# Optimization experiments

Measured on AMD Instinct MI355X. Metric: run time of the kernel, lower is better.

Reference implementation:

```python
import jax, jax.numpy as jnp
import numpy as np
import math

B, N, C = 4, 2048, 768
H = 12
DFF = 4 * C
EPS = 1e-5

def _layernorm(x, gamma, beta):
    mu = jnp.mean(x, axis=-1, keepdims=True)
    var = jnp.var(x, axis=-1, keepdims=True)
    return (x - mu) * jax.lax.rsqrt(var + EPS) * gamma + beta

def setup_inputs() -> dict:
    key = jax.random.key(0)
    ks = jax.random.split(key, 12)
    s = 0.02
    return {
        "x": jax.random.normal(ks[0], (B, N, C), jnp.float32),
        "Wqkv": jax.random.normal(ks[1], (C, 3 * C), jnp.float32) * s,
        "bqkv": jnp.zeros((3 * C,), jnp.float32),
        "Wproj": jax.random.normal(ks[2], (C, C), jnp.float32) * s,
        "bproj": jnp.zeros((C,), jnp.float32),
        "g1": jnp.ones((C,), jnp.float32),
        "b1": jnp.zeros((C,), jnp.float32),
        "g2": jnp.ones((C,), jnp.float32),
        "b2": jnp.zeros((C,), jnp.float32),
        "Wfc1": jax.random.normal(ks[3], (C, DFF), jnp.float32) * s,
        "bfc1": jnp.zeros((DFF,), jnp.float32),
        "Wfc2": jax.random.normal(ks[4], (DFF, C), jnp.float32) * s,
        "bfc2": jnp.zeros((C,), jnp.float32),
    }

def reference(x, Wqkv, bqkv, Wproj, bproj, g1, b1, g2, b2, Wfc1, bfc1, Wfc2, bfc2):
    head_dim = C // H
    qkv = x @ Wqkv + bqkv                      # [B,N,3C]
    q, k, v = jnp.split(qkv, 3, axis=-1)
    # [B,N,C] -> [B,H,N,hd]
    def to_heads(t):
        return t.reshape(B, N, H, head_dim).transpose(0, 2, 1, 3)
    q, k, v = to_heads(q), to_heads(k), to_heads(v)
    attn = jnp.einsum('bhqd,bhkd->bhqk', q, k) / math.sqrt(head_dim)
    attn = jax.nn.softmax(attn, axis=-1)       # dropout p=0 -> identity
    out = jnp.einsum('bhqk,bhkd->bhqd', attn, v)
    out = out.transpose(0, 2, 1, 3).reshape(B, N, C)
    out = out @ Wproj + bproj
    x = _layernorm(x + out, g1, b1)
    h = jax.nn.gelu(x @ Wfc1 + bfc1, approximate=False) @ Wfc2 + bfc2
    x = _layernorm(x + h, g2, b2)
    return x
```

## Files before the change

### kernel.cpp

```cpp
#include <hip/hip_runtime.h>

typedef __bf16 bf16;
typedef __bf16 bf16x2 __attribute__((ext_vector_type(2)));
typedef __bf16 bf16x4 __attribute__((ext_vector_type(4)));
typedef __bf16 bf16x8 __attribute__((ext_vector_type(8)));
typedef float  f32x4  __attribute__((ext_vector_type(4)));
typedef float  f32x16 __attribute__((ext_vector_type(16)));
typedef int    intx4  __attribute__((ext_vector_type(4)));

#define BB 4
#define SEQ 2048
#define CH 768
#define NH 12
#define HD 64
#define DFF 3072
#define MROWS (BB * SEQ)
#define C3 (3 * CH)

__device__ inline f32x16 mfma32(bf16x8 a, bf16x8 b, f32x16 c) {
    return __builtin_amdgcn_mfma_f32_32x32x16_bf16(a, b, c, 0, 0, 0);
}
__device__ inline f32x4 mfma16(bf16x8 a, bf16x8 b, f32x4 c) {
    return __builtin_amdgcn_mfma_f32_16x16x32_bf16(a, b, c, 0, 0, 0);
}
__device__ inline void gload16(const void* g, void* l) {
    __builtin_amdgcn_global_load_lds((const __attribute__((address_space(1))) void*)g,
                                     (__attribute__((address_space(3))) void*)l, 16, 0, 0);
}

__global__ void cvt_f32_bf16(const float* __restrict__ in, bf16* __restrict__ out, int n) {
    int i = (blockIdx.x * blockDim.x + threadIdx.x) * 4;
    if (i + 3 >= n) {
        for (int j = 0; j < 4 && i + j < n; ++j) out[i + j] = (bf16)in[i + j];
        return;
    }
    f32x4 v = *(const f32x4*)&in[i];
    bf16x4 o;
    #pragma unroll
    for (int j = 0; j < 4; ++j) o[j] = (bf16)v[j];
    *(bf16x4*)&out[i] = o;
}

__global__ void transpose_cvt(const float* __restrict__ in, bf16* __restrict__ out, int R, int Cc) {
    __shared__ bf16 t[32][33];
    int tx = threadIdx.x & 31, ty = threadIdx.x >> 5;
    int c0 = blockIdx.x * 32, r0 = blockIdx.y * 32;
    #pragma unroll
    for (int i = 0; i < 32; i += 8)
        t[ty + i][tx] = (bf16)in[(size_t)(r0 + ty + i) * Cc + c0 + tx];
    __syncthreads();
    #pragma unroll
    for (int i = 0; i < 32; i += 8)
        out[(size_t)(c0 + ty + i) * R + r0 + tx] = t[tx][ty + i];
}

__global__ void transpose_v(const bf16* __restrict__ qkvb, bf16* __restrict__ vt) {
    __shared__ bf16 t[32][33];
    int tx = threadIdx.x & 31, ty = threadIdx.x >> 5;
    int n0 = blockIdx.x * 32, d0 = blockIdx.y * 32, bh = blockIdx.z;
    int b = bh / NH, h = bh - b * NH;
    #pragma unroll
    for (int i = 0; i < 32; i += 8)
        t[ty + i][tx] = qkvb[((size_t)b * SEQ + n0 + ty + i) * C3 + 2 * CH + h * HD + d0 + tx];
    __syncthreads();
    #pragma unroll
    for (int i = 0; i < 32; i += 8)
        vt[((size_t)bh * HD + d0 + ty + i) * SEQ + n0 + tx] = t[tx][ty + i];
}

template <int OMODE>
__global__ __launch_bounds__(256) void gemm_bt(const bf16* __restrict__ A,
                                               const bf16* __restrict__ Bt,
                                               const float* __restrict__ bias,
                                               void* __restrict__ Cout,
                                               int M, int N, int K, int lda) {
    __shared__ __align__(16) bf16 As[128][32];
    __shared__ __align__(16) bf16 Bs[128][32];
    const int nwg = gridDim.x * gridDim.y;
    const int orig = blockIdx.y * gridDim.x + blockIdx.x;
    const int wg = (orig & 7) * (nwg >> 3) + (orig >> 3);
    const int bm = (wg / gridDim.x) * 128, bn = (wg % gridDim.x) * 128;
    const int kbeg = blockIdx.z * K;
    const int tid = threadIdx.x;
    const int lane = tid & 63, w = tid >> 6;
    const int wr = w >> 1, wc = w & 1;
    const int lr = lane & 15, lg = lane >> 4;

    const int srow = tid >> 2, schk = (tid & 3) * 8;
    const bf16* gA0 = A + (size_t)(bm + srow) * lda + kbeg + schk;
    const bf16* gA1 = A + (size_t)(bm + 64 + srow) * lda + kbeg + schk;
    const bf16* gB0 = Bt + (size_t)(bn + srow) * lda + kbeg + schk;
    const bf16* gB1 = Bt + (size_t)(bn + 64 + srow) * lda + kbeg + schk;
    bf16* lA0 = &As[srow][schk];
    bf16* lA1 = &As[64 + srow][schk];
    bf16* lB0 = &Bs[srow][schk];
    bf16* lB1 = &Bs[64 + srow][schk];

    f32x4 acc[4][4];
    #pragma unroll
    for (int i = 0; i < 4; ++i)
        #pragma unroll
        for (int j = 0; j < 4; ++j) acc[i][j] = (f32x4){0.f, 0.f, 0.f, 0.f};

    for (int k0 = 0; k0 < K; k0 += 32) {
        __syncthreads();
        gload16(gA0, lA0); gload16(gA1, lA1);
        gload16(gB0, lB0); gload16(gB1, lB1);
        gA0 += 32; gA1 += 32; gB0 += 32; gB1 += 32;
        __syncthreads();
        bf16x8 af[4], bfr[4];
        #pragma unroll
        for (int mi = 0; mi < 4; ++mi)
            af[mi] = *(const bf16x8*)&As[wr * 64 + mi * 16 + lr][lg * 8];
        #pragma unroll
        for (int ni = 0; ni < 4; ++ni)
            bfr[ni] = *(const bf16x8*)&Bs[wc * 64 + ni * 16 + lr][lg * 8];
        #pragma unroll
        for (int mi = 0; mi < 4; ++mi)
            #pragma unroll
            for (int ni = 0; ni < 4; ++ni)
                acc[mi][ni] = mfma16(af[mi], bfr[ni], acc[mi][ni]);
    }

    float* outp = (float*)Cout;
    if (OMODE == 3) outp += (size_t)blockIdx.z * M * N;

    #pragma unroll
    for (int mi = 0; mi < 4; ++mi) {
        #pragma unroll
        for (int ni = 0; ni < 4; ++ni) {
            int col = bn + wc * 64 + ni * 16 + lr;
            float bsv = (OMODE == 3) ? 0.f : bias[col];
            #pragma unroll
            for (int r = 0; r < 4; ++r) {
                int row = bm + wr * 64 + mi * 16 + lg * 4 + r;
                float v = acc[mi][ni][r] + bsv;
                if (OMODE == 2) v = 0.5f * v * (1.0f + erff(v * 0.70710678118654752f));
                if (OMODE == 0 || OMODE == 3)
                    outp[(size_t)row * N + col] = v;
                else
                    ((bf16*)Cout)[(size_t)row * N + col] = (bf16)v;
            }
        }
    }
}

#define C2F 0.18033688011112f
#define THR2 11.5416f
__global__ __launch_bounds__(256, 3) void attn_kernel(const bf16* __restrict__ qkvb,
                                                      const bf16* __restrict__ vt,
                                                      bf16* __restrict__ outb) {
    __shared__ __align__(16) bf16 Kl[2][64 * 64];
    __shared__ __align__(16) bf16 Vl[2][64 * 64];
    const int tid = threadIdx.x;
    const int w = tid >> 6, lane = tid & 63;
    const int lq = lane & 31;
    const int hi = lane >> 5;
    const int lin = blockIdx.x;
    const int xcd = lin & 7, slot = lin >> 3;
    const int bh = xcd * 6 + (slot >> 4);
    const int qt = slot & 15;
    const int b = bh / NH, h = bh - b * NH;
    const int q0 = qt * 128 + w * 32;

    const bf16* qbase = qkvb + (size_t)b * SEQ * C3 + h * HD;
    const bf16* kbase = qbase + CH;
    const bf16* vbase = vt + (size_t)bh * HD * SEQ;

    const int srow = tid >> 3;
    const int ksc = (tid & 7) ^ (srow & 7);
    const bf16* gk0 = kbase + (size_t)srow * C3 + ksc * 8;
    const bf16* gk1 = kbase + (size_t)(srow + 32) * C3 + ksc * 8;
    const bf16* gv0 = vbase + (size_t)srow * SEQ + ksc * 8;
    const bf16* gv1 = vbase + (size_t)(srow + 32) * SEQ + ksc * 8;
    const int ldst = tid * 8;

    bf16x8 qf[4];
    #pragma unroll
    for (int ks = 0; ks < 4; ++ks)
        qf[ks] = *(const bf16x8*)&qbase[(size_t)(q0 + lq) * C3 + ks * 16 + hi * 8];

    f32x16 o0 = {0.f}, o1 = {0.f};
    float m = -3.0e38f, l = 0.f;

    const int swz = lq & 7;

    auto stage = [&](int buf, int kv0) {
        gload16(gk0 + (size_t)kv0 * C3, &Kl[buf][ldst]);
        gload16(gk1 + (size_t)kv0 * C3, &Kl[buf][2048 + ldst]);
        gload16(gv0 + kv0, &Vl[buf][ldst]);
        gload16(gv1 + kv0, &Vl[buf][2048 + ldst]);
    };

    auto process = [&](const bf16* Kb, const bf16* Vb) {
        f32x16 st0 = {0.f}, st1 = {0.f};
        #pragma unroll
        for (int ks = 0; ks < 4; ++ks) {
            int c = 8 * ((2 * ks + hi) ^ swz);
            bf16x8 k0 = *(const bf16x8*)&Kb[lq * 64 + c];
            bf16x8 k1 = *(const bf16x8*)&Kb[(32 + lq) * 64 + c];
            st0 = mfma32(k0, qf[ks], st0);
            st1 = mfma32(k1, qf[ks], st1);
        }
        float t_[8];
        #pragma unroll
        for (int r = 0; r < 8; ++r)
            t_[r] = fmaxf(fmaxf(st0[r], st0[r + 8]), fmaxf(st1[r], st1[r + 8]));
        #pragma unroll
        for (int r = 0; r < 4; ++r) t_[r] = fmaxf(t_[r], t_[r + 4]);
        float mx = fmaxf(fmaxf(t_[0], t_[1]), fmaxf(t_[2], t_[3]));
        mx = fmaxf(mx, __shfl_xor(mx, 32));
        float m2x = mx * C2F;
        if (!__all(m2x <= m + THR2)) {
            float mn = fmaxf(m, m2x);
            float alpha = __builtin_amdgcn_exp2f(m - mn);
            m = mn;
            l *= alpha;
            #pragma unroll
            for (int r = 0; r < 16; ++r) {
                int qr = (r & 3) + 8 * (r >> 2) + 4 * hi;
                float ar = __shfl(alpha, qr);
                o0[r] *= ar;
                o1[r] *= ar;
            }
        }
        bf16x8 pa[4];
        float ps0, ps1;
        {
            float p[16];
            #pragma unroll
            for (int r = 0; r < 16; ++r) p[r] = __builtin_amdgcn_exp2f(fmaf(st0[r], C2F, -m));
            float s0[8];
            #pragma unroll
            for (int r = 0; r < 8; ++r) s0[r] = p[r] + p[r + 8];
            #pragma unroll
            for (int r = 0; r < 4; ++r) s0[r] += s0[r + 4];
            ps0 = (s0[0] + s0[1]) + (s0[2] + s0[3]);
            int a[8];
            #pragma unroll
            for (int i = 0; i < 8; ++i) {
                bf16x2 t2 = {(bf16)p[2 * i], (bf16)p[2 * i + 1]};
                a[i] = __builtin_bit_cast(int, t2);
            }
            int d0 = __shfl_xor(hi ? a[0] : a[2], 32);
            int d1 = __shfl_xor(hi ? a[1] : a[3], 32);
            int d2 = __shfl_xor(hi ? a[4] : a[6], 32);
            int d3 = __shfl_xor(hi ? a[5] : a[7], 32);
            intx4 f0 = hi ? (intx4){d0, d1, a[2], a[3]} : (intx4){a[0], a[1], d0, d1};
            intx4 f1 = hi ? (intx4){d2, d3, a[6], a[7]} : (intx4){a[4], a[5], d2, d3};
            pa[0] = __builtin_bit_cast(bf16x8, f0);
            pa[1] = __builtin_bit_cast(bf16x8, f1);
        }
        {
            float p[16];
            #pragma unroll
            for (int r = 0; r < 16; ++r) p[r] = __builtin_amdgcn_exp2f(fmaf(st1[r], C2F, -m));
            float s0[8];
            #pragma unroll
            for (int r = 0; r < 8; ++r) s0[r] = p[r] + p[r + 8];
            #pragma unroll
            for (int r = 0; r < 4; ++r) s0[r] += s0[r + 4];
            ps1 = (s0[0] + s0[1]) + (s0[2] + s0[3]);
            int a[8];
            #pragma unroll
            for (int i = 0; i < 8; ++i) {
                bf16x2 t2 = {(bf16)p[2 * i], (bf16)p[2 * i + 1]};
                a[i] = __builtin_bit_cast(int, t2);
            }
            int d0 = __shfl_xor(hi ? a[0] : a[2], 32);
            int d1 = __shfl_xor(hi ? a[1] : a[3], 32);
            int d2 = __shfl_xor(hi ? a[4] : a[6], 32);
            int d3 = __shfl_xor(hi ? a[5] : a[7], 32);
            intx4 f0 = hi ? (intx4){d0, d1, a[2], a[3]} : (intx4){a[0], a[1], d0, d1};
            intx4 f1 = hi ? (intx4){d2, d3, a[6], a[7]} : (intx4){a[4], a[5], d2, d3};
            pa[2] = __builtin_bit_cast(bf16x8, f0);
            pa[3] = __builtin_bit_cast(bf16x8, f1);
        }
        float ps = ps0 + ps1;
        ps += __shfl_xor(ps, 32);
        l += ps;
        #pragma unroll
        for (int c = 0; c < 4; ++c) {
            int cc = 8 * ((2 * c + hi) ^ swz);
            bf16x8 v0 = *(const bf16x8*)&Vb[lq * 64 + cc];
            bf16x8 v1 = *(const bf16x8*)&Vb[(32 + lq) * 64 + cc];
            o0 = mfma32(pa[c], v0, o0);
            o1 = mfma32(pa[c], v1, o1);
        }
    };

    stage(0, 0);
    __syncthreads();
    for (int t = 0; t < 32; t += 2) {
        stage(1, (t + 1) * 64);
        process(Kl[0], Vl[0]);
        __syncthreads();
        stage(0, (t + 2 < 32 ? t + 2 : 31) * 64);
        process(Kl[1], Vl[1]);
        __syncthreads();
    }

    float linv = 1.0f / l;
    const size_t obase = (size_t)b * SEQ * CH + h * HD;
    #pragma unroll
    for (int r = 0; r < 16; ++r) {
        int qr = (r & 3) + 8 * (r >> 2) + 4 * hi;
        float lr_ = __shfl(linv, qr);
        size_t rowo = obase + (size_t)(q0 + qr) * CH;
        outb[rowo + lq] = (bf16)(o0[r] * lr_);
        outb[rowo + 32 + lq] = (bf16)(o1[r] * lr_);
    }
}

__global__ __launch_bounds__(256) void add_ln(const float* __restrict__ x,
                                              const float* __restrict__ t0,
                                              const float* __restrict__ t1,
                                              const float* __restrict__ bias,
                                              const float* __restrict__ g,
                                              const float* __restrict__ bt,
                                              float* __restrict__ y,
                                              bf16* __restrict__ yb) {
    const int row = blockIdx.x;
    const size_t base = (size_t)row * CH;
    const int tid = threadIdx.x;
    float v[3];
    #pragma unroll
    for (int k = 0; k < 3; ++k) {
        int c = tid + k * 256;
        float acc = x[base + c] + t0[base + c];
        if (t1) acc += t1[base + c];
        if (bias) acc += bias[c];
        v[k] = acc;
    }
    __shared__ float red[4];
    float s = v[0] + v[1] + v[2];
    #pragma unroll
    for (int off = 32; off >= 1; off >>= 1) s += __shfl_down(s, off);
    if ((tid & 63) == 0) red[tid >> 6] = s;
    __syncthreads();
    float mean = (red[0] + red[1] + red[2] + red[3]) * (1.0f / 768.0f);
    float q = 0.f;
    #pragma unroll
    for (int k = 0; k < 3; ++k) {
        float d = v[k] - mean;
        q += d * d;
    }
    __syncthreads();
    #pragma unroll
    for (int off = 32; off >= 1; off >>= 1) q += __shfl_down(q, off);
    if ((tid & 63) == 0) red[tid >> 6] = q;
    __syncthreads();
    float var = (red[0] + red[1] + red[2] + red[3]) * (1.0f / 768.0f);
    float rstd = rsqrtf(var + 1e-5f);
    #pragma unroll
    for (int k = 0; k < 3; ++k) {
        int c = tid + k * 256;
        float out = (v[k] - mean) * rstd * g[c] + bt[c];
        y[base + c] = out;
        if (yb) yb[base + c] = (bf16)out;
    }
}

extern "C" void kernel_launch(void* const* d_in, const int* in_sizes, int n_in,
                              void* d_out, int out_size, void* d_ws, size_t ws_size,
                              hipStream_t stream) {
    const float* x    = (const float*)d_in[0];
    const float* Wqkv = (const float*)d_in[1];
    const float* bqkv = (const float*)d_in[2];
    const float* Wproj= (const float*)d_in[3];
    const float* bproj= (const float*)d_in[4];
    const float* g1   = (const float*)d_in[5];
    const float* b1   = (const float*)d_in[6];
    const float* g2   = (const float*)d_in[7];
    const float* b2   = (const float*)d_in[8];
    const float* Wfc1 = (const float*)d_in[9];
    const float* bfc1 = (const float*)d_in[10];
    const float* Wfc2 = (const float*)d_in[11];
    const float* bfc2 = (const float*)d_in[12];

    char* ws = (char*)d_ws;
    size_t off = 0;
    auto alloc = [&](size_t bytes) -> void* {
        void* p = ws + off;
        off += (bytes + 255) & ~(size_t)255;
        return p;
    };

    bf16* xb     = (bf16*)alloc((size_t)MROWS * CH * 2);
    bf16* WqkvT  = (bf16*)alloc((size_t)C3 * CH * 2);
    bf16* WprojT = (bf16*)alloc((size_t)CH * CH * 2);
    bf16* Wfc1T  = (bf16*)alloc((size_t)DFF * CH * 2);
    bf16* Wfc2T  = (bf16*)alloc((size_t)CH * DFF * 2);
    bf16* qkvb   = (bf16*)alloc((size_t)MROWS * C3 * 2);
    bf16* vtb    = (bf16*)alloc((size_t)BB * NH * HD * SEQ * 2);
    bf16* attnb  = (bf16*)alloc((size_t)MROWS * CH * 2);
    float* tmpP  = (float*)alloc((size_t)2 * MROWS * CH * 4);
    float* y1    = (float*)alloc((size_t)MROWS * CH * 4);
    bf16* y1b    = (bf16*)alloc((size_t)MROWS * CH * 2);
    bf16* hb     = (bf16*)alloc((size_t)MROWS * DFF * 2);

    cvt_f32_bf16<<<(MROWS * CH / 4 + 255) / 256, 256, 0, stream>>>(x, xb, MROWS * CH);
    transpose_cvt<<<dim3(C3 / 32, CH / 32), 256, 0, stream>>>(Wqkv, WqkvT, CH, C3);
    transpose_cvt<<<dim3(CH / 32, CH / 32), 256, 0, stream>>>(Wproj, WprojT, CH, CH);
    transpose_cvt<<<dim3(DFF / 32, CH / 32), 256, 0, stream>>>(Wfc1, Wfc1T, CH, DFF);
    transpose_cvt<<<dim3(CH / 32, DFF / 32), 256, 0, stream>>>(Wfc2, Wfc2T, DFF, CH);
    gemm_bt<1><<<dim3(C3 / 128, MROWS / 128), 256, 0, stream>>>(xb, WqkvT, bqkv, qkvb, MROWS, C3, CH, CH);
    transpose_v<<<dim3(SEQ / 32, HD / 32, BB * NH), 256, 0, stream>>>(qkvb, vtb);
    attn_kernel<<<768, 256, 0, stream>>>(qkvb, vtb, attnb);
    gemm_bt<3><<<dim3(CH / 128, MROWS / 128, 2), 256, 0, stream>>>(attnb, WprojT, nullptr, tmpP, MROWS, CH, CH / 2, CH);
    add_ln<<<MROWS, 256, 0, stream>>>(x, tmpP, tmpP + (size_t)MROWS * CH, bproj, g1, b1, y1, y1b);
    gemm_bt<2><<<dim3(DFF / 128, MROWS / 128), 256, 0, stream>>>(y1b, Wfc1T, bfc1, hb, MROWS, DFF, CH, CH);
    gemm_bt<3><<<dim3(CH / 128, MROWS / 128, 2), 256, 0, stream>>>(hb, Wfc2T, nullptr, tmpP, MROWS, CH, DFF / 2, DFF);
    add_ln<<<MROWS, 256, 0, stream>>>(y1, tmpP, tmpP + (size_t)MROWS * CH, bfc2, g2, b2, (float*)d_out, nullptr);
}
```

Before: 339.7 us.

## Double-buffer GEMM LDS tiles and tune attention max reduction and priorities

```diff
diff --git a/kernel.cpp b/kernel.cpp
--- a/kernel.cpp
+++ b/kernel.cpp
@@ -74,8 +74,8 @@
                                                const float* __restrict__ bias,
                                                void* __restrict__ Cout,
                                                int M, int N, int K, int lda) {
-    __shared__ __align__(16) bf16 As[128][32];
-    __shared__ __align__(16) bf16 Bs[128][32];
+    __shared__ __align__(16) bf16 As[2][128][32];
+    __shared__ __align__(16) bf16 Bs[2][128][32];
     const int nwg = gridDim.x * gridDim.y;
     const int orig = blockIdx.y * gridDim.x + blockIdx.x;
     const int wg = (orig & 7) * (nwg >> 3) + (orig >> 3);
@@ -91,10 +91,13 @@
     const bf16* gA1 = A + (size_t)(bm + 64 + srow) * lda + kbeg + schk;
     const bf16* gB0 = Bt + (size_t)(bn + srow) * lda + kbeg + schk;
     const bf16* gB1 = Bt + (size_t)(bn + 64 + srow) * lda + kbeg + schk;
-    bf16* lA0 = &As[srow][schk];
-    bf16* lA1 = &As[64 + srow][schk];
-    bf16* lB0 = &Bs[srow][schk];
-    bf16* lB1 = &Bs[64 + srow][schk];
+
+    auto stage = [&](int buf, int kofs) {
+        gload16(gA0 + kofs, &As[buf][srow][schk]);
+        gload16(gA1 + kofs, &As[buf][64 + srow][schk]);
+        gload16(gB0 + kofs, &Bs[buf][srow][schk]);
+        gload16(gB1 + kofs, &Bs[buf][64 + srow][schk]);
+    };
 
     f32x4 acc[4][4];
     #pragma unroll
@@ -102,24 +105,24 @@
         #pragma unroll
         for (int j = 0; j < 4; ++j) acc[i][j] = (f32x4){0.f, 0.f, 0.f, 0.f};
 
+    stage(0, 0);
+    int cur = 0;
     for (int k0 = 0; k0 < K; k0 += 32) {
         __syncthreads();
-        gload16(gA0, lA0); gload16(gA1, lA1);
-        gload16(gB0, lB0); gload16(gB1, lB1);
-        gA0 += 32; gA1 += 32; gB0 += 32; gB1 += 32;
-        __syncthreads();
+        if (k0 + 32 < K) stage(cur ^ 1, k0 + 32);
         bf16x8 af[4], bfr[4];
         #pragma unroll
         for (int mi = 0; mi < 4; ++mi)
-            af[mi] = *(const bf16x8*)&As[wr * 64 + mi * 16 + lr][lg * 8];
+            af[mi] = *(const bf16x8*)&As[cur][wr * 64 + mi * 16 + lr][lg * 8];
         #pragma unroll
         for (int ni = 0; ni < 4; ++ni)
-            bfr[ni] = *(const bf16x8*)&Bs[wc * 64 + ni * 16 + lr][lg * 8];
+            bfr[ni] = *(const bf16x8*)&Bs[cur][wc * 64 + ni * 16 + lr][lg * 8];
         #pragma unroll
         for (int mi = 0; mi < 4; ++mi)
             #pragma unroll
             for (int ni = 0; ni < 4; ++ni)
                 acc[mi][ni] = mfma16(af[mi], bfr[ni], acc[mi][ni]);
+        cur ^= 1;
     }
 
     float* outp = (float*)Cout;
@@ -194,6 +197,7 @@
 
     auto process = [&](const bf16* Kb, const bf16* Vb) {
         f32x16 st0 = {0.f}, st1 = {0.f};
+        __builtin_amdgcn_s_setprio(1);
         #pragma unroll
         for (int ks = 0; ks < 4; ++ks) {
             int c = 8 * ((2 * ks + hi) ^ swz);
@@ -202,17 +206,26 @@
             st0 = mfma32(k0, qf[ks], st0);
             st1 = mfma32(k1, qf[ks], st1);
         }
-        float t_[8];
-        #pragma unroll
-        for (int r = 0; r < 8; ++r)
-            t_[r] = fmaxf(fmaxf(st0[r], st0[r + 8]), fmaxf(st1[r], st1[r + 8]));
-        #pragma unroll
-        for (int r = 0; r < 4; ++r) t_[r] = fmaxf(t_[r], t_[r + 4]);
-        float mx = fmaxf(fmaxf(t_[0], t_[1]), fmaxf(t_[2], t_[3]));
-        mx = fmaxf(mx, __shfl_xor(mx, 32));
-        float m2x = mx * C2F;
-        if (!__all(m2x <= m + THR2)) {
-            float mn = fmaxf(m, m2x);
+        __builtin_amdgcn_s_setprio(0);
+        float a0 = fmaxf(fmaxf(st0[0], st0[1]), st0[2]);
+        float a1 = fmaxf(fmaxf(st0[3], st0[4]), st0[5]);
+        float a2 = fmaxf(fmaxf(st0[6], st0[7]), st0[8]);
+        float a3 = fmaxf(fmaxf(st0[9], st0[10]), st0[11]);
+        float a4 = fmaxf(fmaxf(st0[12], st0[13]), st0[14]);
+        float a5 = fmaxf(fmaxf(st0[15], st1[0]), st1[1]);
+        float a6 = fmaxf(fmaxf(st1[2], st1[3]), st1[4]);
+        float a7 = fmaxf(fmaxf(st1[5], st1[6]), st1[7]);
+        float a8 = fmaxf(fmaxf(st1[8], st1[9]), st1[10]);
+        float a9 = fmaxf(fmaxf(st1[11], st1[12]), st1[13]);
+        float a10 = fmaxf(st1[14], st1[15]);
+        float b0 = fmaxf(fmaxf(a0, a1), a2);
+        float b1 = fmaxf(fmaxf(a3, a4), a5);
+        float b2 = fmaxf(fmaxf(a6, a7), a8);
+        float lmax = fmaxf(fmaxf(b0, b1), fmaxf(b2, fmaxf(a9, a10)));
+        float l2x = lmax * C2F;
+        if (!__all(l2x <= m + THR2)) {
+            float mx = fmaxf(lmax, __shfl_xor(lmax, 32));
+            float mn = fmaxf(m, mx * C2F);
             float alpha = __builtin_amdgcn_exp2f(m - mn);
             m = mn;
             l *= alpha;
@@ -279,6 +292,7 @@
         float ps = ps0 + ps1;
         ps += __shfl_xor(ps, 32);
         l += ps;
+        __builtin_amdgcn_s_setprio(1);
         #pragma unroll
         for (int c = 0; c < 4; ++c) {
             int cc = 8 * ((2 * c + hi) ^ swz);
@@ -287,6 +301,7 @@
             o0 = mfma32(pa[c], v0, o0);
             o1 = mfma32(pa[c], v1, o1);
         }
+        __builtin_amdgcn_s_setprio(0);
     };
 
     stage(0, 0);
```

After: 335.0 us. No clear change (-1.4%).

## Double-buffer GEMM LDS, store split-K partials and residual in bf16, use permlane swaps

Applied to the files above, without the earlier changes.

```diff
diff --git a/kernel.cpp b/kernel.cpp
--- a/kernel.cpp
+++ b/kernel.cpp
@@ -27,6 +27,14 @@
     __builtin_amdgcn_global_load_lds((const __attribute__((address_space(1))) void*)g,
                                      (__attribute__((address_space(3))) void*)l, 16, 0, 0);
 }
+__device__ inline void plswap_i(int& x, int& y) {
+    asm volatile("v_permlane32_swap_b32 %0, %1" : "+v"(x), "+v"(y));
+}
+__device__ inline void plswap_f(float& x, float& y) {
+    asm volatile("v_permlane32_swap_b32 %0, %1" : "+v"(x), "+v"(y));
+}
+__device__ inline int bcast_lo(int v) { int x = v, y = v; plswap_i(x, y); return y; }
+__device__ inline int bcast_hi(int v) { int x = v, y = v; plswap_i(x, y); return x; }
 
 __global__ void cvt_f32_bf16(const float* __restrict__ in, bf16* __restrict__ out, int n) {
     int i = (blockIdx.x * blockDim.x + threadIdx.x) * 4;
@@ -74,8 +82,8 @@
                                                const float* __restrict__ bias,
                                                void* __restrict__ Cout,
                                                int M, int N, int K, int lda) {
-    __shared__ __align__(16) bf16 As[128][32];
-    __shared__ __align__(16) bf16 Bs[128][32];
+    __shared__ __align__(16) bf16 As[2][128][32];
+    __shared__ __align__(16) bf16 Bs[2][128][32];
     const int nwg = gridDim.x * gridDim.y;
     const int orig = blockIdx.y * gridDim.x + blockIdx.x;
     const int wg = (orig & 7) * (nwg >> 3) + (orig >> 3);
@@ -91,10 +99,13 @@
     const bf16* gA1 = A + (size_t)(bm + 64 + srow) * lda + kbeg + schk;
     const bf16* gB0 = Bt + (size_t)(bn + srow) * lda + kbeg + schk;
     const bf16* gB1 = Bt + (size_t)(bn + 64 + srow) * lda + kbeg + schk;
-    bf16* lA0 = &As[srow][schk];
-    bf16* lA1 = &As[64 + srow][schk];
-    bf16* lB0 = &Bs[srow][schk];
-    bf16* lB1 = &Bs[64 + srow][schk];
+
+    auto stage = [&](int buf, int kofs) {
+        gload16(gA0 + kofs, &As[buf][srow][schk]);
+        gload16(gA1 + kofs, &As[buf][64 + srow][schk]);
+        gload16(gB0 + kofs, &Bs[buf][srow][schk]);
+        gload16(gB1 + kofs, &Bs[buf][64 + srow][schk]);
+    };
 
     f32x4 acc[4][4];
     #pragma unroll
@@ -102,28 +113,25 @@
         #pragma unroll
         for (int j = 0; j < 4; ++j) acc[i][j] = (f32x4){0.f, 0.f, 0.f, 0.f};
 
+    stage(0, 0);
+    int cur = 0;
     for (int k0 = 0; k0 < K; k0 += 32) {
         __syncthreads();
-        gload16(gA0, lA0); gload16(gA1, lA1);
-        gload16(gB0, lB0); gload16(gB1, lB1);
-        gA0 += 32; gA1 += 32; gB0 += 32; gB1 += 32;
-        __syncthreads();
+        if (k0 + 32 < K) stage(cur ^ 1, k0 + 32);
         bf16x8 af[4], bfr[4];
         #pragma unroll
         for (int mi = 0; mi < 4; ++mi)
-            af[mi] = *(const bf16x8*)&As[wr * 64 + mi * 16 + lr][lg * 8];
+            af[mi] = *(const bf16x8*)&As[cur][wr * 64 + mi * 16 + lr][lg * 8];
         #pragma unroll
         for (int ni = 0; ni < 4; ++ni)
-            bfr[ni] = *(const bf16x8*)&Bs[wc * 64 + ni * 16 + lr][lg * 8];
+            bfr[ni] = *(const bf16x8*)&Bs[cur][wc * 64 + ni * 16 + lr][lg * 8];
         #pragma unroll
         for (int mi = 0; mi < 4; ++mi)
             #pragma unroll
             for (int ni = 0; ni < 4; ++ni)
                 acc[mi][ni] = mfma16(af[mi], bfr[ni], acc[mi][ni]);
-    }
-
-    float* outp = (float*)Cout;
-    if (OMODE == 3) outp += (size_t)blockIdx.z * M * N;
+        cur ^= 1;
+    }
 
     #pragma unroll
     for (int mi = 0; mi < 4; ++mi) {
@@ -136,8 +144,10 @@
                 int row = bm + wr * 64 + mi * 16 + lg * 4 + r;
                 float v = acc[mi][ni][r] + bsv;
                 if (OMODE == 2) v = 0.5f * v * (1.0f + erff(v * 0.70710678118654752f));
-                if (OMODE == 0 || OMODE == 3)
-                    outp[(size_t)row * N + col] = v;
+                if (OMODE == 0)
+                    ((float*)Cout)[(size_t)row * N + col] = v;
+                else if (OMODE == 3)
+                    ((bf16*)Cout)[(size_t)blockIdx.z * M * N + (size_t)row * N + col] = (bf16)v;
                 else
                     ((bf16*)Cout)[(size_t)row * N + col] = (bf16)v;
             }
@@ -208,9 +218,10 @@
             t_[r] = fmaxf(fmaxf(st0[r], st0[r + 8]), fmaxf(st1[r], st1[r + 8]));
         #pragma unroll
         for (int r = 0; r < 4; ++r) t_[r] = fmaxf(t_[r], t_[r + 4]);
-        float mx = fmaxf(fmaxf(t_[0], t_[1]), fmaxf(t_[2], t_[3]));
-        mx = fmaxf(mx, __shfl_xor(mx, 32));
-        float m2x = mx * C2F;
+        float lmax = fmaxf(fmaxf(t_[0], t_[1]), fmaxf(t_[2], t_[3]));
+        float mxa = lmax, mxb = lmax;
+        plswap_f(mxa, mxb);
+        float m2x = fmaxf(mxa, mxb) * C2F;
         if (!__all(m2x <= m + THR2)) {
             float mn = fmaxf(m, m2x);
             float alpha = __builtin_amdgcn_exp2f(m - mn);
@@ -242,12 +253,8 @@
                 bf16x2 t2 = {(bf16)p[2 * i], (bf16)p[2 * i + 1]};
                 a[i] = __builtin_bit_cast(int, t2);
             }
-            int d0 = __shfl_xor(hi ? a[0] : a[2], 32);
-            int d1 = __shfl_xor(hi ? a[1] : a[3], 32);
-            int d2 = __shfl_xor(hi ? a[4] : a[6], 32);
-            int d3 = __shfl_xor(hi ? a[5] : a[7], 32);
-            intx4 f0 = hi ? (intx4){d0, d1, a[2], a[3]} : (intx4){a[0], a[1], d0, d1};
-            intx4 f1 = hi ? (intx4){d2, d3, a[6], a[7]} : (intx4){a[4], a[5], d2, d3};
+            intx4 f0 = {bcast_lo(a[0]), bcast_lo(a[1]), bcast_hi(a[2]), bcast_hi(a[3])};
+            intx4 f1 = {bcast_lo(a[4]), bcast_lo(a[5]), bcast_hi(a[6]), bcast_hi(a[7])};
             pa[0] = __builtin_bit_cast(bf16x8, f0);
             pa[1] = __builtin_bit_cast(bf16x8, f1);
         }
@@ -267,18 +274,15 @@
                 bf16x2 t2 = {(bf16)p[2 * i], (bf16)p[2 * i + 1]};
                 a[i] = __builtin_bit_cast(int, t2);
             }
-            int d0 = __shfl_xor(hi ? a[0] : a[2], 32);
-            int d1 = __shfl_xor(hi ? a[1] : a[3], 32);
-            int d2 = __shfl_xor(hi ? a[4] : a[6], 32);
-            int d3 = __shfl_xor(hi ? a[5] : a[7], 32);
-            intx4 f0 = hi ? (intx4){d0, d1, a[2], a[3]} : (intx4){a[0], a[1], d0, d1};
-            intx4 f1 = hi ? (intx4){d2, d3, a[6], a[7]} : (intx4){a[4], a[5], d2, d3};
+            intx4 f0 = {bcast_lo(a[0]), bcast_lo(a[1]), bcast_hi(a[2]), bcast_hi(a[3])};
+            intx4 f1 = {bcast_lo(a[4]), bcast_lo(a[5]), bcast_hi(a[6]), bcast_hi(a[7])};
             pa[2] = __builtin_bit_cast(bf16x8, f0);
             pa[3] = __builtin_bit_cast(bf16x8, f1);
         }
         float ps = ps0 + ps1;
-        ps += __shfl_xor(ps, 32);
-        l += ps;
+        float pa_ = ps, pb_ = ps;
+        plswap_f(pa_, pb_);
+        l += pa_ + pb_;
         #pragma unroll
         for (int c = 0; c < 4; ++c) {
             int cc = 8 * ((2 * c + hi) ^ swz);
@@ -312,14 +316,14 @@
     }
 }
 
-__global__ __launch_bounds__(256) void add_ln(const float* __restrict__ x,
-                                              const float* __restrict__ t0,
-                                              const float* __restrict__ t1,
+template <int XBF16, int OUTF32>
+__global__ __launch_bounds__(256) void add_ln(const void* __restrict__ xin,
+                                              const bf16* __restrict__ t0,
+                                              const bf16* __restrict__ t1,
                                               const float* __restrict__ bias,
                                               const float* __restrict__ g,
                                               const float* __restrict__ bt,
-                                              float* __restrict__ y,
-                                              bf16* __restrict__ yb) {
+                                              void* __restrict__ yout) {
     const int row = blockIdx.x;
     const size_t base = (size_t)row * CH;
     const int tid = threadIdx.x;
@@ -327,10 +331,9 @@
     #pragma unroll
     for (int k = 0; k < 3; ++k) {
         int c = tid + k * 256;
-        float acc = x[base + c] + t0[base + c];
-        if (t1) acc += t1[base + c];
-        if (bias) acc += bias[c];
-        v[k] = acc;
+        float xv = XBF16 ? (float)((const bf16*)xin)[base + c]
+                         : ((const float*)xin)[base + c];
+        v[k] = xv + (float)t0[base + c] + (float)t1[base + c] + bias[c];
     }
     __shared__ float red[4];
     float s = v[0] + v[1] + v[2];
@@ -356,8 +359,8 @@
     for (int k = 0; k < 3; ++k) {
         int c = tid + k * 256;
         float out = (v[k] - mean) * rstd * g[c] + bt[c];
-        y[base + c] = out;
-        if (yb) yb[base + c] = (bf16)out;
+        if (OUTF32) ((float*)yout)[base + c] = out;
+        else        ((bf16*)yout)[base + c] = (bf16)out;
     }
 }
 
@@ -394,8 +397,7 @@
     bf16* qkvb   = (bf16*)alloc((size_t)MROWS * C3 * 2);
     bf16* vtb    = (bf16*)alloc((size_t)BB * NH * HD * SEQ * 2);
     bf16* attnb  = (bf16*)alloc((size_t)MROWS * CH * 2);
-    float* tmpP  = (float*)alloc((size_t)2 * MROWS * CH * 4);
-    float* y1    = (float*)alloc((size_t)MROWS * CH * 4);
+    bf16* tmpP   = (bf16*)alloc((size_t)2 * MROWS * CH * 2);
     bf16* y1b    = (bf16*)alloc((size_t)MROWS * CH * 2);
     bf16* hb     = (bf16*)alloc((size_t)MROWS * DFF * 2);
 
@@ -408,8 +410,8 @@
     transpose_v<<<dim3(SEQ / 32, HD / 32, BB * NH), 256, 0, stream>>>(qkvb, vtb);
     attn_kernel<<<768, 256, 0, stream>>>(qkvb, vtb, attnb);
     gemm_bt<3><<<dim3(CH / 128, MROWS / 128, 2), 256, 0, stream>>>(attnb, WprojT, nullptr, tmpP, MROWS, CH, CH / 2, CH);
-    add_ln<<<MROWS, 256, 0, stream>>>(x, tmpP, tmpP + (size_t)MROWS * CH, bproj, g1, b1, y1, y1b);
+    add_ln<0, 0><<<MROWS, 256, 0, stream>>>(x, tmpP, tmpP + (size_t)MROWS * CH, bproj, g1, b1, y1b);
     gemm_bt<2><<<dim3(DFF / 128, MROWS / 128), 256, 0, stream>>>(y1b, Wfc1T, bfc1, hb, MROWS, DFF, CH, CH);
     gemm_bt<3><<<dim3(CH / 128, MROWS / 128, 2), 256, 0, stream>>>(hb, Wfc2T, nullptr, tmpP, MROWS, CH, DFF / 2, DFF);
-    add_ln<<<MROWS, 256, 0, stream>>>(y1, tmpP, tmpP + (size_t)MROWS * CH, bfc2, g2, b2, (float*)d_out, nullptr);
-}
+    add_ln<1, 1><<<MROWS, 256, 0, stream>>>(y1b, tmpP, tmpP + (size_t)MROWS * CH, bfc2, g2, b2, (float*)d_out);
+}
```

Result: faster. 302.0 us (-11.1%).
